# Optimization experiments

Hardware: AMD Instinct MI355X
Metric: run time of the kernel (lower is better)

Reference implementation:

```python
import jax, jax.numpy as jnp
import numpy as np

N, HID, HEADS = 50000, 256, 8
D = HID // HEADS  # per-head dim = 32
E = 800000


def setup_inputs() -> dict:
    key = jax.random.key(0)
    ks = jax.random.split(key, 12)
    s = 0.02
    x = jax.random.normal(ks[0], (N, HID), dtype=jnp.float32)
    edge_index = jax.random.randint(ks[1], (2, E), 0, N, dtype=jnp.int64)
    # TransformerConv params (PyG defaults: root_weight=True, concat=True, beta=False)
    Wq = jax.random.normal(ks[2], (HID, HID), dtype=jnp.float32) * s
    bq = jnp.zeros((HID,), dtype=jnp.float32)
    Wk = jax.random.normal(ks[3], (HID, HID), dtype=jnp.float32) * s
    bk = jnp.zeros((HID,), dtype=jnp.float32)
    Wv = jax.random.normal(ks[4], (HID, HID), dtype=jnp.float32) * s
    bv = jnp.zeros((HID,), dtype=jnp.float32)
    Wskip = jax.random.normal(ks[5], (HID, HID), dtype=jnp.float32) * s
    bskip = jnp.zeros((HID,), dtype=jnp.float32)
    gamma = jnp.ones((HID,), dtype=jnp.float32)
    beta = jnp.zeros((HID,), dtype=jnp.float32)
    return {"x": x, "edge_index": edge_index, "Wq": Wq, "bq": bq, "Wk": Wk,
            "bk": bk, "Wv": Wv, "bv": bv, "Wskip": Wskip, "bskip": bskip,
            "gamma": gamma, "beta": beta}


def _gnn_layer(x, edge_index, Wq, bq, Wk, bk, Wv, bv, Wskip, bskip, gamma, beta):
    n = x.shape[0]
    src, dst = edge_index[0], edge_index[1]  # messages flow src(j) -> dst(i)
    q = (x @ Wq + bq).reshape(n, HEADS, D)
    k = (x @ Wk + bk).reshape(n, HEADS, D)
    v = (x @ Wv + bv).reshape(n, HEADS, D)
    # per-edge attention logits [E, HEADS]
    logits = jnp.einsum('ehd,ehd->eh', q[dst], k[src]) / jnp.sqrt(jnp.float32(D))
    # segment softmax over destination neighborhoods (stable)
    seg_max = jax.ops.segment_max(logits, dst, num_segments=n)  # [N, HEADS]
    expv = jnp.exp(logits - seg_max[dst])
    denom = jax.ops.segment_sum(expv, dst, num_segments=n)
    attn = expv / denom[dst]  # [E, HEADS]  (dropout in eval mode -> identity)
    # scatter-aggregate weighted values, concat heads
    agg = jax.ops.segment_sum(attn[:, :, None] * v[src], dst, num_segments=n)
    out = agg.reshape(n, HID) + (x @ Wskip + bskip)  # root/skip connection
    h = jax.nn.gelu(out, approximate=False)
    # residual + LayerNorm
    y = x + h
    mu = jnp.mean(y, axis=-1, keepdims=True)
    var = jnp.var(y, axis=-1, keepdims=True)
    return (y - mu) / jnp.sqrt(var + 1e-5) * gamma + beta


def reference(x, edge_index, Wq, bq, Wk, bk, Wv, bv, Wskip, bskip, gamma, beta):
    return _gnn_layer(x, edge_index, Wq, bq, Wk, bk, Wv, bv, Wskip, bskip, gamma, beta)
```

## Files before the change

kernel.cpp:

```cpp
#include <hip/hip_runtime.h>

#define N_NODES 50000
#define HID 256
#define HEADS 8
#define HDIM 32
#define N_EDGES 800000

typedef __bf16 bf16x8 __attribute__((ext_vector_type(8)));
typedef float f32x4 __attribute__((ext_vector_type(4)));
typedef float f32x2 __attribute__((ext_vector_type(2)));

__device__ __forceinline__ unsigned short f2bf(float f) {
    unsigned int b = __float_as_uint(f);
    unsigned int r = (b + 0x7FFFu + ((b >> 16) & 1u)) >> 16;
    return (unsigned short)r;
}
__device__ __forceinline__ float bf2f(unsigned short u) {
    return __uint_as_float(((unsigned int)u) << 16);
}
__device__ __forceinline__ f32x2 bfpair(unsigned int u) {
    f32x2 r;
    r[0] = __uint_as_float(u << 16);
    r[1] = __uint_as_float(u & 0xffff0000u);
    return r;
}

__device__ __forceinline__ void fused_col_map(int p, int& mat, int& col, float& scale) {
    if (p < 256) { mat = 0; col = p; scale = 1.0f; }
    else if (p < 768) {
        int pp = p - 256;
        mat = ((pp & 2) ? 2 : 1);
        col = ((pp >> 2) << 1) | (pp & 1);
        scale = 64.0f;
    } else { mat = 3; col = p - 768; scale = 1.0f; }
}

__global__ __launch_bounds__(256) void prep_kernel(
    const float* __restrict__ x, unsigned short* __restrict__ xb,
    const int* __restrict__ dst, int* __restrict__ deg,
    const float* __restrict__ Wq, const float* __restrict__ Wk,
    const float* __restrict__ Wv, const float* __restrict__ Ws,
    const float* __restrict__ bq, const float* __restrict__ bk,
    const float* __restrict__ bv, const float* __restrict__ bs,
    unsigned short* __restrict__ wpack, float* __restrict__ biasF) {
    int b = blockIdx.x;
    if (b < 6250) {
        int t = b * 256 + threadIdx.x;
        const float4* p = reinterpret_cast<const float4*>(x) + (size_t)t * 2;
        float4 f0 = p[0], f1 = p[1];
        uint4 o;
        o.x = (unsigned)f2bf(f0.x) | ((unsigned)f2bf(f0.y) << 16);
        o.y = (unsigned)f2bf(f0.z) | ((unsigned)f2bf(f0.w) << 16);
        o.z = (unsigned)f2bf(f1.x) | ((unsigned)f2bf(f1.y) << 16);
        o.w = (unsigned)f2bf(f1.z) | ((unsigned)f2bf(f1.w) << 16);
        reinterpret_cast<uint4*>(xb)[t] = o;
    } else if (b < 9375) {
        int e = (b - 6250) * 256 + threadIdx.x;
        atomicAdd(&deg[dst[e]], 1);
    } else {
        int t = (b - 9375) * 256 + threadIdx.x;
        int e = t & 7, lane = (t >> 3) & 63, kk = (t >> 9) & 7, n_tile = t >> 12;
        int k = kk * 32 + (lane >> 4) * 8 + e;
        int p = n_tile * 16 + (lane & 15);
        const float* W[4] = {Wq, Wk, Wv, Ws};
        int mat, col; float scale;
        fused_col_map(p, mat, col, scale);
        wpack[t] = f2bf(W[mat][k * 256 + col] * scale);
        if (t < 1024) {
            const float* B[4] = {bq, bk, bv, bs};
            int mat2, col2; float s2;
            fused_col_map(t, mat2, col2, s2);
            biasF[t] = B[mat2][col2] * s2;
        }
    }
}

__global__ __launch_bounds__(1024) void scan1_kernel(
    const int* __restrict__ deg, int* __restrict__ row_ptr,
    int* __restrict__ btot, int n) {
    int tid = threadIdx.x, lane = tid & 63, wv = tid >> 6;
    int idx = blockIdx.x * 1024 + tid;
    int v = (idx < n) ? deg[idx] : 0;
    int inc = v;
#pragma unroll
    for (int off = 1; off < 64; off <<= 1) {
        int t2 = __shfl_up(inc, off);
        if (lane >= off) inc += t2;
    }
    __shared__ int sW[16], sO[16];
    if (lane == 63) sW[wv] = inc;
    __syncthreads();
    if (tid < 16) {
        int vv = sW[tid], in2 = vv;
        for (int off = 1; off < 16; off <<= 1) {
            int t2 = __shfl_up(in2, off);
            if (tid >= off) in2 += t2;
        }
        sO[tid] = in2 - vv;
    }
    __syncthreads();
    int excl = sO[wv] + inc - v;
    if (idx <= n) row_ptr[idx] = excl;
    if (tid == 1023) btot[blockIdx.x] = excl + v;
}

__global__ __launch_bounds__(256) void fixup_kernel(
    int* __restrict__ row_ptr, int* __restrict__ fill,
    const int* __restrict__ btot, int n) {
    __shared__ int sB;
    int tid = threadIdx.x;
    if (tid < 64) {
        int v = (tid < 50) ? btot[tid] : 0;
        int inc = v;
#pragma unroll
        for (int off = 1; off < 64; off <<= 1) {
            int t2 = __shfl_up(inc, off);
            if (tid >= off) inc += t2;
        }
        if (tid == (blockIdx.x >> 2)) sB = inc - v;
    }
    __syncthreads();
    int idx = blockIdx.x * 256 + tid;
    if (idx > n) return;
    int v = row_ptr[idx] + sB;
    row_ptr[idx] = v;
    if (idx < n) fill[idx] = v;
}

__global__ __launch_bounds__(256) void gemm_scatter_kernel(
    const int* __restrict__ src, const int* __restrict__ dst,
    int* __restrict__ fill, int* __restrict__ csr_src,
    const unsigned short* __restrict__ xb,
    const unsigned short* __restrict__ wpack,
    const float* __restrict__ biasF,
    unsigned char* __restrict__ qkvs,
    int n_nodes) {
    int b = blockIdx.x;
    if (b < 3125) {
        int e = b * 256 + threadIdx.x;
        if (e < N_EDGES) {
            int pos = atomicAdd(&fill[dst[e]], 1);
            csr_src[pos] = src[e];
        }
        return;
    }
    int gid = b - 3125;
    int work = (gid & 7) * 782 + (gid >> 3);
    int mt = work >> 4;
    int nt = work & 15;
    int lane = threadIdx.x & 63;
    int wv = threadIdx.x >> 6;
    int row_w = mt * 128 + wv * 32;
    int n0 = nt * 64;

    f32x4 acc[2][4];
#pragma unroll
    for (int mi = 0; mi < 2; ++mi)
#pragma unroll
        for (int ni = 0; ni < 4; ++ni) {
            f32x4 z = {0.f, 0.f, 0.f, 0.f};
            acc[mi][ni] = z;
        }

    int arow0 = min(row_w + (lane & 15), n_nodes - 1);
    int arow1 = min(row_w + 16 + (lane & 15), n_nodes - 1);
    int acol = (lane >> 4) * 8;
    const uint4* bbase = reinterpret_cast<const uint4*>(wpack);
    int ntile0 = n0 >> 4;

#pragma unroll
    for (int kk = 0; kk < 8; ++kk) {
        bf16x8 a[2], bfr[4];
        {
            uint4 u0 = *reinterpret_cast<const uint4*>(xb + (size_t)arow0 * 256 + kk * 32 + acol);
            uint4 u1 = *reinterpret_cast<const uint4*>(xb + (size_t)arow1 * 256 + kk * 32 + acol);
            a[0] = __builtin_bit_cast(bf16x8, u0);
            a[1] = __builtin_bit_cast(bf16x8, u1);
        }
#pragma unroll
        for (int ni = 0; ni < 4; ++ni) {
            uint4 u = bbase[((size_t)(ntile0 + ni) * 8 + kk) * 64 + lane];
            bfr[ni] = __builtin_bit_cast(bf16x8, u);
        }
#pragma unroll
        for (int mi = 0; mi < 2; ++mi)
#pragma unroll
            for (int ni = 0; ni < 4; ++ni)
                acc[mi][ni] = __builtin_amdgcn_mfma_f32_16x16x32_bf16(
                    a[mi], bfr[ni], acc[mi][ni], 0, 0, 0);
    }

    int region = (n0 < 256) ? 0 : (n0 < 768 ? 1 : 2);
#pragma unroll
    for (int mi = 0; mi < 2; ++mi) {
        int rbase = row_w + mi * 16 + (lane >> 4) * 4;
#pragma unroll
        for (int ni = 0; ni < 4; ++ni) {
            int col = n0 + ni * 16 + (lane & 15);
            float bias = biasF[col];
#pragma unroll
            for (int r = 0; r < 4; ++r) {
                int row = rbase + r;
                if (row < n_nodes) {
                    float val = acc[mi][ni][r] + bias;
                    size_t rb = (size_t)row * 1536;
                    if (region == 0) {
                        *reinterpret_cast<unsigned short*>(qkvs + rb + col * 2) = f2bf(val);
                    } else if (region == 1) {
                        int p8 = __builtin_amdgcn_cvt_pk_fp8_f32(val, val, 0, false);
                        qkvs[rb + 512 + (col - 256)] = (unsigned char)(p8 & 0xff);
                    } else {
                        *reinterpret_cast<unsigned short*>(qkvs + rb + 1024 + (col - 768) * 2) = f2bf(val);
                    }
                }
            }
        }
    }
}

__global__ __launch_bounds__(256) void edge_agg_kernel(
    const int* __restrict__ row_ptr, const int* __restrict__ csr_src,
    const unsigned char* __restrict__ qkvs, const unsigned short* __restrict__ xb,
    const float* __restrict__ gamma, const float* __restrict__ beta,
    float* __restrict__ out) {
    int wv = threadIdx.x >> 6;
    int i = blockIdx.x * 4 + wv;
    int lane = threadIdx.x & 63;
    int half = lane >> 5, l = lane & 31;

    const float QS = 0.17677669529663687f * 1.4426950408889634f / 64.0f;
    const unsigned char* rowi = qkvs + (unsigned)i * 1536u;
    uint4 qu = *reinterpret_cast<const uint4*>(rowi + l * 16);
    f32x2 qsc = {QS, QS};
    f32x2 q01 = bfpair(qu.x) * qsc;
    f32x2 q23 = bfpair(qu.y) * qsc;
    f32x2 q45 = bfpair(qu.z) * qsc;
    f32x2 q67 = bfpair(qu.w) * qsc;

    int e0 = row_ptr[i], e1 = row_ptr[i + 1];
    f32x2 acc0 = {0.f, 0.f}, acc1 = {0.f, 0.f}, acc2 = {0.f, 0.f}, acc3 = {0.f, 0.f};
    float den = 0.f;
    int e = e0 + half;
    int j = (e < e1) ? csr_src[e] : 0;
    while (e < e1) {
        int jn = (e + 2 < e1) ? csr_src[e + 2] : 0;
        uint4 u = *reinterpret_cast<const uint4*>(
            qkvs + (unsigned)j * 1536u + 512u + (unsigned)l * 16u);
        f32x2 k01 = __builtin_amdgcn_cvt_pk_f32_fp8(u.x, false);
        f32x2 v01 = __builtin_amdgcn_cvt_pk_f32_fp8(u.x, true);
        f32x2 k23 = __builtin_amdgcn_cvt_pk_f32_fp8(u.y, false);
        f32x2 v23 = __builtin_amdgcn_cvt_pk_f32_fp8(u.y, true);
        f32x2 k45 = __builtin_amdgcn_cvt_pk_f32_fp8(u.z, false);
        f32x2 v45 = __builtin_amdgcn_cvt_pk_f32_fp8(u.z, true);
        f32x2 k67 = __builtin_amdgcn_cvt_pk_f32_fp8(u.w, false);
        f32x2 v67 = __builtin_amdgcn_cvt_pk_f32_fp8(u.w, true);
        f32x2 d = q01 * k01;
        d = __builtin_elementwise_fma(q23, k23, d);
        d = __builtin_elementwise_fma(q45, k45, d);
        d = __builtin_elementwise_fma(q67, k67, d);
        float s = d[0] + d[1];
        s += __shfl_xor(s, 1);
        s += __shfl_xor(s, 2);
        float w = exp2f(s);
        den += w;
        f32x2 w2 = {w, w};
        acc0 = __builtin_elementwise_fma(w2, v01, acc0);
        acc1 = __builtin_elementwise_fma(w2, v23, acc1);
        acc2 = __builtin_elementwise_fma(w2, v45, acc2);
        acc3 = __builtin_elementwise_fma(w2, v67, acc3);
        j = jn;
        e += 2;
    }

    acc0[0] += __shfl_xor(acc0[0], 32); acc0[1] += __shfl_xor(acc0[1], 32);
    acc1[0] += __shfl_xor(acc1[0], 32); acc1[1] += __shfl_xor(acc1[1], 32);
    acc2[0] += __shfl_xor(acc2[0], 32); acc2[1] += __shfl_xor(acc2[1], 32);
    acc3[0] += __shfl_xor(acc3[0], 32); acc3[1] += __shfl_xor(acc3[1], 32);
    den += __shfl_xor(den, 32);
    float inv = (den > 0.f) ? 1.0f / (den * 64.0f) : 0.f;

    uint4 su = *reinterpret_cast<const uint4*>(rowi + 1024 + l * 16);
    uint4 xu = *reinterpret_cast<const uint4*>(xb + (size_t)i * 256 + l * 8);
    const float C1 = -2.3022650556f;
    const float C2 = -0.10294578f;
    float s1 = 0.f, s2 = 0.f;
    f32x2 y01, y23, y45, y67;
#define GNN_PROC(A, SRAW, XRAW, Y)                                   \
    {                                                                \
        f32x2 skp = bfpair(SRAW), xr = bfpair(XRAW);                 \
        _Pragma("unroll")                                            \
        for (int qq = 0; qq < 2; ++qq) {                             \
            float pre = fmaf(A[qq], inv, skp[qq]);                   \
            float x2 = pre * pre;                                    \
            float arg = pre * fmaf(C2, x2, C1);                      \
            float gel = pre / (1.f + exp2f(arg));                    \
            float yy = xr[qq] + gel;                                 \
            Y[qq] = yy;                                              \
            s1 += yy;                                                \
            s2 = fmaf(yy, yy, s2);                                   \
        }                                                            \
    }
    GNN_PROC(acc0, su.x, xu.x, y01)
    GNN_PROC(acc1, su.y, xu.y, y23)
    GNN_PROC(acc2, su.z, xu.z, y45)
    GNN_PROC(acc3, su.w, xu.w, y67)
#undef GNN_PROC

#pragma unroll
    for (int m = 1; m <= 16; m <<= 1) {
        s1 += __shfl_xor(s1, m);
        s2 += __shfl_xor(s2, m);
    }
    float mu = s1 * (1.f / 256.f);
    float var = s2 * (1.f / 256.f) - mu * mu;
    float rstd = rsqrtf(var + 1e-5f);

    if (half == 0) {
        const float4* g4 = reinterpret_cast<const float4*>(gamma) + l * 2;
        const float4* b4 = reinterpret_cast<const float4*>(beta) + l * 2;
        float4 ga = g4[0], gb = g4[1], ba = b4[0], bb = b4[1];
        float4 o0, o1;
        o0.x = (y01[0] - mu) * rstd * ga.x + ba.x;
        o0.y = (y01[1] - mu) * rstd * ga.y + ba.y;
        o0.z = (y23[0] - mu) * rstd * ga.z + ba.z;
        o0.w = (y23[1] - mu) * rstd * ga.w + ba.w;
        o1.x = (y45[0] - mu) * rstd * gb.x + bb.x;
        o1.y = (y45[1] - mu) * rstd * gb.y + bb.y;
        o1.z = (y67[0] - mu) * rstd * gb.z + bb.z;
        o1.w = (y67[1] - mu) * rstd * gb.w + bb.w;
        float4* op = reinterpret_cast<float4*>(out + (unsigned)i * 256u + l * 8);
        op[0] = o0;
        op[1] = o1;
    }
}

extern "C" void kernel_launch(void* const* d_in, const int* in_sizes, int n_in,
                              void* d_out, int out_size, void* d_ws, size_t ws_size,
                              hipStream_t stream) {
    const float* x    = (const float*)d_in[0];
    const int*   ei   = (const int*)d_in[1];
    const float* Wq   = (const float*)d_in[2];
    const float* bq   = (const float*)d_in[3];
    const float* Wk   = (const float*)d_in[4];
    const float* bk   = (const float*)d_in[5];
    const float* Wv   = (const float*)d_in[6];
    const float* bv   = (const float*)d_in[7];
    const float* Wsk  = (const float*)d_in[8];
    const float* bsk  = (const float*)d_in[9];
    const float* gamma = (const float*)d_in[10];
    const float* beta  = (const float*)d_in[11];
    const int* src = ei;
    const int* dst = ei + N_EDGES;

    char* ws = (char*)d_ws;
    size_t off = 0;
    auto alloc = [&](size_t bytes) -> void* {
        void* p = ws + off;
        off += (bytes + 255) & ~(size_t)255;
        return p;
    };
    unsigned short* xb     = (unsigned short*)alloc((size_t)N_NODES * 256 * 2);
    unsigned char*  qkvs   = (unsigned char*)alloc((size_t)N_NODES * 1536);
    unsigned short* wpack  = (unsigned short*)alloc(262144 * 2);
    float*          biasF  = (float*)alloc(1024 * 4);
    int*            deg    = (int*)alloc((size_t)N_NODES * 4);
    int*            rowp   = (int*)alloc((size_t)(N_NODES + 1) * 4);
    int*            fill   = (int*)alloc((size_t)N_NODES * 4);
    int*            csr    = (int*)alloc((size_t)N_EDGES * 4);
    int*            btot   = (int*)alloc(64 * 4);
    (void)ws_size;

    hipMemsetAsync(deg, 0, (size_t)N_NODES * 4, stream);
    prep_kernel<<<10399, 256, 0, stream>>>(x, xb, dst, deg, Wq, Wk, Wv, Wsk,
                                           bq, bk, bv, bsk, wpack, biasF);
    scan1_kernel<<<50, 1024, 0, stream>>>(deg, rowp, btot, N_NODES);
    fixup_kernel<<<196, 256, 0, stream>>>(rowp, fill, btot, N_NODES);
    gemm_scatter_kernel<<<9381, 256, 0, stream>>>(src, dst, fill, csr,
                                                  xb, wpack, biasF, qkvs, N_NODES);
    edge_agg_kernel<<<12500, 256, 0, stream>>>(rowp, csr, qkvs, xb, gamma, beta,
                                               (float*)d_out);
}
```

Measured before the change: 258.1 us.

## Split scatter from GEMM, stage weights in LDS, separate Q/KV/skip buffers

Splits the fused edge-scatter + QKV GEMM kernel into two launches. The GEMM now stages each block's 32 KB weight slice in shared memory instead of reading it per wave from global. The packed 1536-byte per-node qkvs row is replaced by separate Q, KV and skip arrays, so the KV rows gathered per edge are densely packed at 512 bytes. This aims to improve cache locality for the random KV gathers and cut redundant weight loads, at the cost of one extra launch and lost overlap between scatter and GEMM.

```diff
diff --git a/kernel.cpp b/kernel.cpp
--- a/kernel.cpp
+++ b/kernel.cpp
@@ -127,31 +127,44 @@
     if (idx < n) fill[idx] = v;
 }
 
-__global__ __launch_bounds__(256) void gemm_scatter_kernel(
+__global__ __launch_bounds__(256) void scatter_kernel(
     const int* __restrict__ src, const int* __restrict__ dst,
-    int* __restrict__ fill, int* __restrict__ csr_src,
+    int* __restrict__ fill, int* __restrict__ csr_src, int ne) {
+    int e = blockIdx.x * 256 + threadIdx.x;
+    if (e < ne) {
+        int pos = atomicAdd(&fill[dst[e]], 1);
+        csr_src[pos] = src[e];
+    }
+}
+
+__global__ __launch_bounds__(256) void gemm_kernel(
     const unsigned short* __restrict__ xb,
     const unsigned short* __restrict__ wpack,
     const float* __restrict__ biasF,
-    unsigned char* __restrict__ qkvs,
+    unsigned short* __restrict__ qs,
+    unsigned char* __restrict__ kv,
+    unsigned short* __restrict__ sk,
     int n_nodes) {
-    int b = blockIdx.x;
-    if (b < 3125) {
-        int e = b * 256 + threadIdx.x;
-        if (e < N_EDGES) {
-            int pos = atomicAdd(&fill[dst[e]], 1);
-            csr_src[pos] = src[e];
-        }
-        return;
-    }
-    int gid = b - 3125;
-    int work = (gid & 7) * 782 + (gid >> 3);
+    __shared__ __align__(16) uint4 bsh[2048];
+    int bid = blockIdx.x;
+    int work = (bid & 7) * 782 + (bid >> 3);
     int mt = work >> 4;
     int nt = work & 15;
     int lane = threadIdx.x & 63;
     int wv = threadIdx.x >> 6;
     int row_w = mt * 128 + wv * 32;
     int n0 = nt * 64;
+    int ntile0 = n0 >> 4;
+
+    {
+        const uint4* bsrc = reinterpret_cast<const uint4*>(wpack) +
+                            (size_t)ntile0 * 8 * 64;
+        int tid = threadIdx.x;
+#pragma unroll
+        for (int i = 0; i < 8; ++i)
+            bsh[i * 256 + tid] = bsrc[i * 256 + tid];
+    }
+    __syncthreads();
 
     f32x4 acc[2][4];
 #pragma unroll
@@ -165,8 +178,6 @@
     int arow0 = min(row_w + (lane & 15), n_nodes - 1);
     int arow1 = min(row_w + 16 + (lane & 15), n_nodes - 1);
     int acol = (lane >> 4) * 8;
-    const uint4* bbase = reinterpret_cast<const uint4*>(wpack);
-    int ntile0 = n0 >> 4;
 
 #pragma unroll
     for (int kk = 0; kk < 8; ++kk) {
@@ -179,7 +190,7 @@
         }
 #pragma unroll
         for (int ni = 0; ni < 4; ++ni) {
-            uint4 u = bbase[((size_t)(ntile0 + ni) * 8 + kk) * 64 + lane];
+            uint4 u = bsh[(ni * 8 + kk) * 64 + lane];
             bfr[ni] = __builtin_bit_cast(bf16x8, u);
         }
 #pragma unroll
@@ -203,14 +214,13 @@
                 int row = rbase + r;
                 if (row < n_nodes) {
                     float val = acc[mi][ni][r] + bias;
-                    size_t rb = (size_t)row * 1536;
                     if (region == 0) {
-                        *reinterpret_cast<unsigned short*>(qkvs + rb + col * 2) = f2bf(val);
+                        qs[(size_t)row * 256 + col] = f2bf(val);
                     } else if (region == 1) {
                         int p8 = __builtin_amdgcn_cvt_pk_fp8_f32(val, val, 0, false);
-                        qkvs[rb + 512 + (col - 256)] = (unsigned char)(p8 & 0xff);
+                        kv[(size_t)row * 512 + (col - 256)] = (unsigned char)(p8 & 0xff);
                     } else {
-                        *reinterpret_cast<unsigned short*>(qkvs + rb + 1024 + (col - 768) * 2) = f2bf(val);
+                        sk[(size_t)row * 256 + (col - 768)] = f2bf(val);
                     }
                 }
             }
@@ -220,7 +230,8 @@
 
 __global__ __launch_bounds__(256) void edge_agg_kernel(
     const int* __restrict__ row_ptr, const int* __restrict__ csr_src,
-    const unsigned char* __restrict__ qkvs, const unsigned short* __restrict__ xb,
+    const unsigned short* __restrict__ qs, const unsigned char* __restrict__ kv,
+    const unsigned short* __restrict__ sk, const unsigned short* __restrict__ xb,
     const float* __restrict__ gamma, const float* __restrict__ beta,
     float* __restrict__ out) {
     int wv = threadIdx.x >> 6;
@@ -229,8 +240,7 @@
     int half = lane >> 5, l = lane & 31;
 
     const float QS = 0.17677669529663687f * 1.4426950408889634f / 64.0f;
-    const unsigned char* rowi = qkvs + (unsigned)i * 1536u;
-    uint4 qu = *reinterpret_cast<const uint4*>(rowi + l * 16);
+    uint4 qu = *reinterpret_cast<const uint4*>(qs + (size_t)i * 256 + l * 8);
     f32x2 qsc = {QS, QS};
     f32x2 q01 = bfpair(qu.x) * qsc;
     f32x2 q23 = bfpair(qu.y) * qsc;
@@ -245,7 +255,7 @@
     while (e < e1) {
         int jn = (e + 2 < e1) ? csr_src[e + 2] : 0;
         uint4 u = *reinterpret_cast<const uint4*>(
-            qkvs + (unsigned)j * 1536u + 512u + (unsigned)l * 16u);
+            kv + (size_t)j * 512u + (unsigned)l * 16u);
         f32x2 k01 = __builtin_amdgcn_cvt_pk_f32_fp8(u.x, false);
         f32x2 v01 = __builtin_amdgcn_cvt_pk_f32_fp8(u.x, true);
         f32x2 k23 = __builtin_amdgcn_cvt_pk_f32_fp8(u.y, false);
@@ -279,7 +289,7 @@
     den += __shfl_xor(den, 32);
     float inv = (den > 0.f) ? 1.0f / (den * 64.0f) : 0.f;
 
-    uint4 su = *reinterpret_cast<const uint4*>(rowi + 1024 + l * 16);
+    uint4 su = *reinterpret_cast<const uint4*>(sk + (size_t)i * 256 + l * 8);
     uint4 xu = *reinterpret_cast<const uint4*>(xb + (size_t)i * 256 + l * 8);
     const float C1 = -2.3022650556f;
     const float C2 = -0.10294578f;
@@ -328,7 +338,7 @@
         o1.y = (y45[1] - mu) * rstd * gb.y + bb.y;
         o1.z = (y67[0] - mu) * rstd * gb.z + bb.z;
         o1.w = (y67[1] - mu) * rstd * gb.w + bb.w;
-        float4* op = reinterpret_cast<float4*>(out + (unsigned)i * 256u + l * 8);
+        float4* op = reinterpret_cast<float4*>(out + (size_t)i * 256 + l * 8);
         op[0] = o0;
         op[1] = o1;
     }
@@ -360,7 +370,9 @@
         return p;
     };
     unsigned short* xb     = (unsigned short*)alloc((size_t)N_NODES * 256 * 2);
-    unsigned char*  qkvs   = (unsigned char*)alloc((size_t)N_NODES * 1536);
+    unsigned short* qs     = (unsigned short*)alloc((size_t)N_NODES * 256 * 2);
+    unsigned char*  kvb    = (unsigned char*)alloc((size_t)N_NODES * 512);
+    unsigned short* sk     = (unsigned short*)alloc((size_t)N_NODES * 256 * 2);
     unsigned short* wpack  = (unsigned short*)alloc(262144 * 2);
     float*          biasF  = (float*)alloc(1024 * 4);
     int*            deg    = (int*)alloc((size_t)N_NODES * 4);
@@ -375,8 +387,8 @@
                                            bq, bk, bv, bsk, wpack, biasF);
     scan1_kernel<<<50, 1024, 0, stream>>>(deg, rowp, btot, N_NODES);
     fixup_kernel<<<196, 256, 0, stream>>>(rowp, fill, btot, N_NODES);
-    gemm_scatter_kernel<<<9381, 256, 0, stream>>>(src, dst, fill, csr,
-                                                  xb, wpack, biasF, qkvs, N_NODES);
-    edge_agg_kernel<<<12500, 256, 0, stream>>>(rowp, csr, qkvs, xb, gamma, beta,
+    scatter_kernel<<<3125, 256, 0, stream>>>(src, dst, fill, csr, N_EDGES);
+    gemm_kernel<<<6256, 256, 0, stream>>>(xb, wpack, biasF, qs, kvb, sk, N_NODES);
+    edge_agg_kernel<<<12500, 256, 0, stream>>>(rowp, csr, qs, kvb, sk, xb, gamma, beta,
                                                (float*)d_out);
 }
```

After: 268.1 us. 3.9% more time.
